# Performance work log

Hardware: AMD Instinct MI355X
Metric: run time of the kernel (lower is better)

## Reference

```python
import jax, jax.numpy as jnp
import numpy as np

EPS = 1e-6
BN_EPS = 1e-5  # torch BatchNorm default eps
B, H, L, D = 4, 8, 128, 64


def _bn(x, gamma, beta, axes):
    # training-mode batchnorm: biased batch stats over `axes`, per-channel (dim 1) affine
    mu = jnp.mean(x, axis=axes, keepdims=True)
    var = jnp.var(x, axis=axes, keepdims=True)
    shape = [1] * x.ndim
    shape[1] = -1
    return (x - mu) * jax.lax.rsqrt(var + BN_EPS) * gamma.reshape(shape) + beta.reshape(shape)


def setup_inputs() -> dict:
    key = jax.random.key(0)
    kq, kk, kv = jax.random.split(key, 3)
    return {
        "Q": jax.random.normal(kq, (B, H, L, D), jnp.float32),
        "K": jax.random.normal(kk, (B, H, L, D), jnp.float32),
        "V": jax.random.uniform(kv, (B, H, L, D), jnp.float32),
        "j_gamma": jnp.ones((H,), jnp.float32),
        "j_beta": jnp.zeros((H,), jnp.float32),
        "h_gamma": jnp.ones((H,), jnp.float32),
        "h_beta": jnp.zeros((H,), jnp.float32),
        "bnH_gamma": jnp.ones((H,), jnp.float32),
        "bnH_beta": jnp.zeros((H,), jnp.float32),
    }


def reference(Q, K, V, j_gamma, j_beta, h_gamma, h_beta, bnH_gamma, bnH_beta):
    # normalize V into a distribution over D, entropy terms
    Vn = V / (jnp.sum(V, axis=-1, keepdims=True) + EPS)
    Vn = jnp.clip(Vn, EPS, 1.0)
    hi = -Vn * jnp.log2(Vn)            # [B,H,L,D]
    h = jnp.sum(hi, axis=-1)           # [B,H,L]

    pQ = jax.nn.softmax(Q, axis=-1)
    pK = jax.nn.softmax(K, axis=-1)
    pQe = pQ[:, :, :, None, :]         # [B,H,L,1,D]
    pKe = pK[:, :, None, :, :]         # [B,H,1,L,D]
    m = 0.5 * (pQe + pKe)              # [B,H,L,L,D] -- dominant intermediate
    kl_q = jnp.sum(pQe * jnp.log2(pQe / (m + EPS) + EPS), axis=-1)  # [B,H,L,L]
    kl_k = jnp.sum(pKe * jnp.log2(pKe / (m + EPS) + EPS), axis=-1)
    J = 0.5 * kl_q + 0.5 * kl_k        # [B,H,L,L]

    # batchnorm only the off-diagonal entries of J (channel = head)
    rows, cols = np.nonzero(~np.eye(L, dtype=bool))
    nd = J[:, :, rows, cols]           # [B,H,L*(L-1)]
    nd = _bn(nd, j_gamma, j_beta, (0, 2))
    J = J.at[:, :, rows, cols].set(nd)

    h = _bn(h, h_gamma, h_beta, (0, 2))

    # QUBO solver stand-in (original detaches + CPU round-trip): binary x per node,
    # greedy heuristic for min x^T J x + h^T x, treated as a constant.
    x = jax.lax.stop_gradient((jnp.sum(J, axis=-1) + h < 0).astype(J.dtype))  # [B,H,L]

    # per-node energy contribution H_i = x_i * ((J x)_i + h_i)
    He = x * (jnp.einsum('bhij,bhj->bhi', J, x) + h)  # [B,H,L]

    Hd = He[..., None] * hi / h[..., None]            # [B,H,L,D]
    Hd = _bn(-Hd, bnH_gamma, bnH_beta, (0, 2, 3))
    return Hd
```

## Files before the change

kernel.cpp:

```cpp
#include <hip/hip_runtime.h>


#define EPS 1e-6f
#define BN_EPS 1e-5f

__global__ void __launch_bounds__(64) k0_rows(
    const float* __restrict__ Q, const float* __restrict__ K,
    const float* __restrict__ V,
    float* __restrict__ pQ, float* __restrict__ pK,
    float* __restrict__ Sq, float* __restrict__ Sk,
    float* __restrict__ hi, float* __restrict__ h_raw)
{
    const int r = blockIdx.x;
    const int lane = threadIdx.x;
    const int base = r * 64 + lane;

    float kk = K[base];
    float m = kk;
    for (int off = 32; off; off >>= 1) m = fmaxf(m, __shfl_xor(m, off));
    float e = __expf(kk - m);
    float s = e;
    for (int off = 32; off; off >>= 1) s += __shfl_xor(s, off);
    const float pk = e * __fdividef(1.0f, s);
    pK[base] = pk;
    float pl = pk * __log2f(pk);
    for (int off = 32; off; off >>= 1) pl += __shfl_xor(pl, off);
    if (lane == 0) Sk[r] = pl;

    float q = Q[base];
    m = q;
    for (int off = 32; off; off >>= 1) m = fmaxf(m, __shfl_xor(m, off));
    e = __expf(q - m);
    s = e;
    for (int off = 32; off; off >>= 1) s += __shfl_xor(s, off);
    const float pq = e * __fdividef(1.0f, s);
    pQ[base] = pq;
    pl = pq * __log2f(pq);
    for (int off = 32; off; off >>= 1) pl += __shfl_xor(pl, off);
    if (lane == 0) Sq[r] = pl;

    float v = V[base];
    s = v;
    for (int off = 32; off; off >>= 1) s += __shfl_xor(s, off);
    float vn = v * __fdividef(1.0f, s + EPS);
    vn = fminf(fmaxf(vn, EPS), 1.0f);
    const float hv = -vn * __log2f(vn);
    hi[base] = hv;
    float hs = hv;
    for (int off = 32; off; off >>= 1) hs += __shfl_xor(hs, off);
    if (lane == 0) h_raw[r] = hs;
}

__global__ void __launch_bounds__(256) ka_J(
    const float* __restrict__ pQ, const float* __restrict__ pK,
    const float* __restrict__ Sq, const float* __restrict__ Sk,
    float* __restrict__ J, float* __restrict__ Sg, float* __restrict__ Dg,
    double* __restrict__ Jpart)
{
    __shared__ float sK[128 * 65];
    __shared__ float sQ[4 * 64];
    __shared__ float sSk[128];
    __shared__ float sSq[4];
    __shared__ double sred[8];
    const int bid = blockIdx.x;
    const int n = bid >> 5;
    const int i0 = (bid & 31) * 4;
    const int tid = threadIdx.x;
    const int wave = tid >> 6, lane = tid & 63;

    const float4* pk4 = (const float4*)(pK + n * 8192);
    #pragma unroll
    for (int v = 0; v < 8; ++v) {
        const int idx = tid + 256 * v;
        const float4 f = pk4[idx];
        float* dst = sK + (idx >> 4) * 65 + (idx & 15) * 4;
        dst[0] = f.x; dst[1] = f.y; dst[2] = f.z; dst[3] = f.w;
    }
    sQ[tid] = pQ[(n * 128 + i0) * 64 + tid];
    if (tid < 128) sSk[tid] = Sk[n * 128 + tid];
    if (tid < 4)   sSq[tid] = Sq[n * 128 + i0 + tid];
    __syncthreads();

    const float* qrow = sQ + wave * 64;
    const float* kp0 = sK + lane * 65;
    const float* kp1 = sK + (lane + 64) * 65;
    float a0 = 0.f, a1 = 0.f;
    #pragma unroll 8
    for (int d = 0; d < 64; ++d) {
        const float qv = qrow[d];
        const float s0v = qv + kp0[d];
        const float s1v = qv + kp1[d];
        a0 += s0v * __log2f(fmaf(0.5f, s0v, EPS));
        a1 += s1v * __log2f(fmaf(0.5f, s1v, EPS));
    }
    const int gi = i0 + wave;
    const float bq = sSq[wave];
    const float J0 = 0.5f * (bq + sSk[lane]      - a0);
    const float J1 = 0.5f * (bq + sSk[lane + 64] - a1);
    const int rbase = (n * 128 + gi) * 128;
    J[rbase + lane] = J0;
    J[rbase + lane + 64] = J1;

    float s0 = J0 + J1;
    for (int off = 32; off; off >>= 1) s0 += __shfl_xor(s0, off);
    const float D = (gi < 64) ? __shfl(J0, gi) : __shfl(J1, gi - 64);
    if (lane == 0) { Sg[n * 128 + gi] = s0; Dg[n * 128 + gi] = D; }

    double ls = 0.0, ls2 = 0.0;
    if (lane != gi)      { ls += J0; ls2 += (double)J0 * (double)J0; }
    if (lane + 64 != gi) { ls += J1; ls2 += (double)J1 * (double)J1; }
    for (int off = 32; off; off >>= 1) {
        ls  += __shfl_xor(ls, off);
        ls2 += __shfl_xor(ls2, off);
    }
    if (lane == 0) { sred[wave] = ls; sred[4 + wave] = ls2; }
    __syncthreads();
    if (tid == 0) {
        Jpart[2 * bid]     = sred[0] + sred[1] + sred[2] + sred[3];
        Jpart[2 * bid + 1] = sred[4] + sred[5] + sred[6] + sred[7];
    }
}

__global__ void __launch_bounds__(256) kc_he(
    const float* __restrict__ J, const float* __restrict__ hi,
    const double* __restrict__ Jpart, const float* __restrict__ h_raw,
    const float* __restrict__ Sg, const float* __restrict__ Dg,
    const float* __restrict__ j_gamma, const float* __restrict__ j_beta,
    const float* __restrict__ h_gamma, const float* __restrict__ h_beta,
    float* __restrict__ t, double* __restrict__ tpart)
{
    __shared__ float sx[128], shbn[128];
    __shared__ double sred[8];
    __shared__ float sprm[5];
    const int bid = blockIdx.x;
    const int n = bid >> 4;
    const int i0 = (bid & 15) * 8;
    const int hh = n & 7;
    const int tid = threadIdx.x;
    const int wave = tid >> 6, lane = tid & 63;

    if (wave == 0) {
        const int p1 = lane, p2 = lane + 64;
        const int pb1 = ((p1 >> 5) * 8 + hh) * 32 + (p1 & 31);
        const int pb2 = ((p2 >> 5) * 8 + hh) * 32 + (p2 & 31);
        double s = Jpart[2 * pb1] + Jpart[2 * pb2];
        double s2 = Jpart[2 * pb1 + 1] + Jpart[2 * pb2 + 1];
        for (int off = 32; off; off >>= 1) {
            s += __shfl_xor(s, off); s2 += __shfl_xor(s2, off);
        }
        if (lane == 0) {
            const double cnt = 65024.0;
            const double mean = s / cnt;
            const double var = s2 / cnt - mean * mean;
            sprm[0] = (float)mean;
            sprm[1] = (float)(1.0 / sqrt(var + (double)BN_EPS));
        }
    }
    {
        double s = 0.0, s2 = 0.0;
        for (int p = tid; p < 512; p += 256) {
            const int b = p >> 7, l = p & 127;
            const float v = h_raw[(b * 8 + hh) * 128 + l];
            s += v; s2 += (double)v * (double)v;
        }
        for (int off = 32; off; off >>= 1) {
            s += __shfl_xor(s, off); s2 += __shfl_xor(s2, off);
        }
        if (lane == 0) { sred[wave] = s; sred[4 + wave] = s2; }
    }
    __syncthreads();
    if (tid == 0) {
        const double hs = sred[0] + sred[1] + sred[2] + sred[3];
        const double hs2 = sred[4] + sred[5] + sred[6] + sred[7];
        const double hm = hs / 512.0;
        const double hvar = hs2 / 512.0 - hm * hm;
        sprm[2] = (float)hm;
        sprm[3] = (float)(1.0 / sqrt(hvar + (double)BN_EPS));
    }
    __syncthreads();
    const float jm = sprm[0], jinv = sprm[1];
    const float hm = sprm[2], hinv = sprm[3];
    const float jg = j_gamma[hh], jb = j_beta[hh];
    if (tid < 128) {
        const int i = tid;
        const float S = Sg[n * 128 + i], D = Dg[n * 128 + i];
        const float hb = (h_raw[n * 128 + i] - hm) * hinv * h_gamma[hh] + h_beta[hh];
        const float rs = jinv * jg * (S - D - 127.0f * jm) + 127.0f * jb + D;
        sx[i] = (rs + hb < 0.0f) ? 1.0f : 0.0f;
        shbn[i] = hb;
    }
    __syncthreads();
    if (wave == 0) {
        float c = sx[lane] + sx[lane + 64];
        for (int off = 32; off; off >>= 1) c += __shfl_xor(c, off);
        if (lane == 0) sprm[4] = c;
    }
    __syncthreads();
    const float C = sprm[4];
    const int rb = wave;
    for (int rr = 0; rr < 2; ++rr) {
        const int i = i0 + rb + 4 * rr;
        const int r = n * 128 + i;
        float tr = J[r * 128 + lane] * sx[lane] + J[r * 128 + 64 + lane] * sx[lane + 64];
        for (int off = 32; off; off >>= 1) tr += __shfl_xor(tr, off);
        const float xi = sx[i], Di = Dg[r];
        const float dot = jinv * jg * (tr - xi * Di - jm * (C - xi))
                        + jb * (C - xi) + xi * Di;
        const float He = xi * (dot + shbn[i]);
        const float tv = -(He * hi[r * 64 + lane] * __fdividef(1.0f, shbn[i]));
        t[r * 64 + lane] = tv;
        double ds = tv, ds2 = (double)tv * (double)tv;
        for (int off = 32; off; off >>= 1) {
            ds += __shfl_xor(ds, off); ds2 += __shfl_xor(ds2, off);
        }
        if (lane == 0) { tpart[2 * r] = ds; tpart[2 * r + 1] = ds2; }
    }
}

__global__ void __launch_bounds__(256) kd_out(
    const double* __restrict__ tpart, const float* __restrict__ t,
    const float* __restrict__ gamma, const float* __restrict__ beta,
    float* __restrict__ out)
{
    __shared__ double sd[256], sd2[256];
    const int bid = blockIdx.x;
    const int tid = threadIdx.x;
    const int g0 = bid * 512;
    const int hh = (g0 >> 13) & 7;
    double s = 0.0, s2 = 0.0;
    for (int p = tid; p < 512; p += 256) {
        const int b = p >> 7, i = p & 127;
        const int r = (b * 8 + hh) * 128 + i;
        s += tpart[2 * r]; s2 += tpart[2 * r + 1];
    }
    sd[tid] = s; sd2[tid] = s2;
    __syncthreads();
    for (int off = 128; off > 0; off >>= 1) {
        if (tid < off) { sd[tid] += sd[tid + off]; sd2[tid] += sd2[tid + off]; }
        __syncthreads();
    }
    const double mean = sd[0] / 32768.0;
    const double var = sd2[0] / 32768.0 - mean * mean;
    const float tm = (float)mean;
    const float tinv = (float)(1.0 / sqrt(var + (double)BN_EPS));
    const float g = gamma[hh], be = beta[hh];
    out[g0 + tid]       = (t[g0 + tid]       - tm) * tinv * g + be;
    out[g0 + 256 + tid] = (t[g0 + 256 + tid] - tm) * tinv * g + be;
}

extern "C" void kernel_launch(void* const* d_in, const int* in_sizes, int n_in,
                              void* d_out, int out_size, void* d_ws, size_t ws_size,
                              hipStream_t stream) {
    (void)in_sizes; (void)n_in; (void)out_size; (void)ws_size;
    const float* Q = (const float*)d_in[0];
    const float* K = (const float*)d_in[1];
    const float* V = (const float*)d_in[2];
    const float* j_gamma = (const float*)d_in[3];
    const float* j_beta  = (const float*)d_in[4];
    const float* h_gamma = (const float*)d_in[5];
    const float* h_beta  = (const float*)d_in[6];
    const float* bnH_gamma = (const float*)d_in[7];
    const float* bnH_beta  = (const float*)d_in[8];
    float* out = (float*)d_out;

    float* w = (float*)d_ws;
    float*  J     = w;
    float*  hi    = w + 524288;
    float*  t     = w + 786432;
    float*  pQ    = w + 1048576;
    float*  pK    = w + 1310720;
    float*  h_raw = w + 1572864;
    float*  Sq    = w + 1576960;
    float*  Sk    = w + 1581056;
    float*  Sg    = w + 1585152;
    float*  Dg    = w + 1589248;
    double* Jpart = (double*)(w + 1593344);
    double* tpart = (double*)(w + 1597440);

    k0_rows<<<4096, 64, 0, stream>>>(Q, K, V, pQ, pK, Sq, Sk, hi, h_raw);
    ka_J<<<1024, 256, 0, stream>>>(pQ, pK, Sq, Sk, J, Sg, Dg, Jpart);
    kc_he<<<512, 256, 0, stream>>>(J, hi, Jpart, h_raw, Sg, Dg,
                                   j_gamma, j_beta, h_gamma, h_beta, t, tpart);
    kd_out<<<512, 256, 0, stream>>>(tpart, t, bnH_gamma, bnH_beta, out);
}
```

Measured before the change: 94.33 us.

## Fuse Q softmax into J kernel and pre-reduce BN partials per block

```diff
diff --git a/kernel.cpp b/kernel.cpp
--- a/kernel.cpp
+++ b/kernel.cpp
@@ -5,10 +5,8 @@
 #define BN_EPS 1e-5f
 
 __global__ void __launch_bounds__(64) k0_rows(
-    const float* __restrict__ Q, const float* __restrict__ K,
-    const float* __restrict__ V,
-    float* __restrict__ pQ, float* __restrict__ pK,
-    float* __restrict__ Sq, float* __restrict__ Sk,
+    const float* __restrict__ K, const float* __restrict__ V,
+    float* __restrict__ pK, float* __restrict__ Sk,
     float* __restrict__ hi, float* __restrict__ h_raw)
 {
     const int r = blockIdx.x;
@@ -27,18 +25,6 @@
     for (int off = 32; off; off >>= 1) pl += __shfl_xor(pl, off);
     if (lane == 0) Sk[r] = pl;
 
-    float q = Q[base];
-    m = q;
-    for (int off = 32; off; off >>= 1) m = fmaxf(m, __shfl_xor(m, off));
-    e = __expf(q - m);
-    s = e;
-    for (int off = 32; off; off >>= 1) s += __shfl_xor(s, off);
-    const float pq = e * __fdividef(1.0f, s);
-    pQ[base] = pq;
-    pl = pq * __log2f(pq);
-    for (int off = 32; off; off >>= 1) pl += __shfl_xor(pl, off);
-    if (lane == 0) Sq[r] = pl;
-
     float v = V[base];
     s = v;
     for (int off = 32; off; off >>= 1) s += __shfl_xor(s, off);
@@ -52,21 +38,33 @@
 }
 
 __global__ void __launch_bounds__(256) ka_J(
-    const float* __restrict__ pQ, const float* __restrict__ pK,
-    const float* __restrict__ Sq, const float* __restrict__ Sk,
+    const float* __restrict__ Q, const float* __restrict__ pK,
+    const float* __restrict__ Sk,
     float* __restrict__ J, float* __restrict__ Sg, float* __restrict__ Dg,
     double* __restrict__ Jpart)
 {
     __shared__ float sK[128 * 65];
     __shared__ float sQ[4 * 64];
     __shared__ float sSk[128];
-    __shared__ float sSq[4];
     __shared__ double sred[8];
     const int bid = blockIdx.x;
     const int n = bid >> 5;
     const int i0 = (bid & 31) * 4;
     const int tid = threadIdx.x;
     const int wave = tid >> 6, lane = tid & 63;
+    const int gi = i0 + wave;
+    const int R = n * 128 + gi;
+
+    float q = Q[R * 64 + lane];
+    float mq = q;
+    for (int off = 32; off; off >>= 1) mq = fmaxf(mq, __shfl_xor(mq, off));
+    float eq = __expf(q - mq);
+    float sq = eq;
+    for (int off = 32; off; off >>= 1) sq += __shfl_xor(sq, off);
+    const float pq = eq * __fdividef(1.0f, sq);
+    sQ[wave * 64 + lane] = pq;
+    float bq = pq * __log2f(pq);
+    for (int off = 32; off; off >>= 1) bq += __shfl_xor(bq, off);
 
     const float4* pk4 = (const float4*)(pK + n * 8192);
     #pragma unroll
@@ -76,9 +74,7 @@
         float* dst = sK + (idx >> 4) * 65 + (idx & 15) * 4;
         dst[0] = f.x; dst[1] = f.y; dst[2] = f.z; dst[3] = f.w;
     }
-    sQ[tid] = pQ[(n * 128 + i0) * 64 + tid];
     if (tid < 128) sSk[tid] = Sk[n * 128 + tid];
-    if (tid < 4)   sSq[tid] = Sq[n * 128 + i0 + tid];
     __syncthreads();
 
     const float* qrow = sQ + wave * 64;
@@ -93,18 +89,16 @@
         a0 += s0v * __log2f(fmaf(0.5f, s0v, EPS));
         a1 += s1v * __log2f(fmaf(0.5f, s1v, EPS));
     }
-    const int gi = i0 + wave;
-    const float bq = sSq[wave];
     const float J0 = 0.5f * (bq + sSk[lane]      - a0);
     const float J1 = 0.5f * (bq + sSk[lane + 64] - a1);
-    const int rbase = (n * 128 + gi) * 128;
+    const int rbase = R * 128;
     J[rbase + lane] = J0;
     J[rbase + lane + 64] = J1;
 
     float s0 = J0 + J1;
     for (int off = 32; off; off >>= 1) s0 += __shfl_xor(s0, off);
     const float D = (gi < 64) ? __shfl(J0, gi) : __shfl(J1, gi - 64);
-    if (lane == 0) { Sg[n * 128 + gi] = s0; Dg[n * 128 + gi] = D; }
+    if (lane == 0) { Sg[R] = s0; Dg[R] = D; }
 
     double ls = 0.0, ls2 = 0.0;
     if (lane != gi)      { ls += J0; ls2 += (double)J0 * (double)J0; }
@@ -127,10 +121,11 @@
     const float* __restrict__ Sg, const float* __restrict__ Dg,
     const float* __restrict__ j_gamma, const float* __restrict__ j_beta,
     const float* __restrict__ h_gamma, const float* __restrict__ h_beta,
-    float* __restrict__ t, double* __restrict__ tpart)
+    float* __restrict__ t, double* __restrict__ tblk)
 {
     __shared__ float sx[128], shbn[128];
     __shared__ double sred[8];
+    __shared__ double st1[4], st2[4];
     __shared__ float sprm[5];
     const int bid = blockIdx.x;
     const int n = bid >> 4;
@@ -198,6 +193,7 @@
     __syncthreads();
     const float C = sprm[4];
     const int rb = wave;
+    double bs = 0.0, bs2 = 0.0;
     for (int rr = 0; rr < 2; ++rr) {
         const int i = i0 + rb + 4 * rr;
         const int r = n * 128 + i;
@@ -213,34 +209,38 @@
         for (int off = 32; off; off >>= 1) {
             ds += __shfl_xor(ds, off); ds2 += __shfl_xor(ds2, off);
         }
-        if (lane == 0) { tpart[2 * r] = ds; tpart[2 * r + 1] = ds2; }
+        if (lane == 0) { bs += ds; bs2 += ds2; }
+    }
+    if (lane == 0) { st1[wave] = bs; st2[wave] = bs2; }
+    __syncthreads();
+    if (tid == 0) {
+        tblk[2 * bid]     = st1[0] + st1[1] + st1[2] + st1[3];
+        tblk[2 * bid + 1] = st2[0] + st2[1] + st2[2] + st2[3];
     }
 }
 
 __global__ void __launch_bounds__(256) kd_out(
-    const double* __restrict__ tpart, const float* __restrict__ t,
+    const double* __restrict__ tblk, const float* __restrict__ t,
     const float* __restrict__ gamma, const float* __restrict__ beta,
     float* __restrict__ out)
 {
-    __shared__ double sd[256], sd2[256];
+    __shared__ double sm[2];
     const int bid = blockIdx.x;
     const int tid = threadIdx.x;
     const int g0 = bid * 512;
     const int hh = (g0 >> 13) & 7;
-    double s = 0.0, s2 = 0.0;
-    for (int p = tid; p < 512; p += 256) {
-        const int b = p >> 7, i = p & 127;
-        const int r = (b * 8 + hh) * 128 + i;
-        s += tpart[2 * r]; s2 += tpart[2 * r + 1];
-    }
-    sd[tid] = s; sd2[tid] = s2;
-    __syncthreads();
-    for (int off = 128; off > 0; off >>= 1) {
-        if (tid < off) { sd[tid] += sd[tid + off]; sd2[tid] += sd2[tid + off]; }
-        __syncthreads();
-    }
-    const double mean = sd[0] / 32768.0;
-    const double var = sd2[0] / 32768.0 - mean * mean;
+    if (tid < 64) {
+        const int b = tid >> 4, tile = tid & 15;
+        const int cb = ((b * 8 + hh) << 4) + tile;
+        double s = tblk[2 * cb], s2 = tblk[2 * cb + 1];
+        for (int off = 32; off; off >>= 1) {
+            s += __shfl_xor(s, off); s2 += __shfl_xor(s2, off);
+        }
+        if (tid == 0) { sm[0] = s; sm[1] = s2; }
+    }
+    __syncthreads();
+    const double mean = sm[0] / 32768.0;
+    const double var = sm[1] / 32768.0 - mean * mean;
     const float tm = (float)mean;
     const float tinv = (float)(1.0 / sqrt(var + (double)BN_EPS));
     const float g = gamma[hh], be = beta[hh];
@@ -267,19 +267,17 @@
     float*  J     = w;
     float*  hi    = w + 524288;
     float*  t     = w + 786432;
-    float*  pQ    = w + 1048576;
     float*  pK    = w + 1310720;
     float*  h_raw = w + 1572864;
-    float*  Sq    = w + 1576960;
     float*  Sk    = w + 1581056;
     float*  Sg    = w + 1585152;
     float*  Dg    = w + 1589248;
     double* Jpart = (double*)(w + 1593344);
-    double* tpart = (double*)(w + 1597440);
-
-    k0_rows<<<4096, 64, 0, stream>>>(Q, K, V, pQ, pK, Sq, Sk, hi, h_raw);
-    ka_J<<<1024, 256, 0, stream>>>(pQ, pK, Sq, Sk, J, Sg, Dg, Jpart);
+    double* tblk  = (double*)(w + 1597440);
+
+    k0_rows<<<4096, 64, 0, stream>>>(K, V, pK, Sk, hi, h_raw);
+    ka_J<<<1024, 256, 0, stream>>>(Q, pK, Sk, J, Sg, Dg, Jpart);
     kc_he<<<512, 256, 0, stream>>>(J, hi, Jpart, h_raw, Sg, Dg,
-                                   j_gamma, j_beta, h_gamma, h_beta, t, tpart);
-    kd_out<<<512, 256, 0, stream>>>(tpart, t, bnH_gamma, bnH_beta, out);
-}
+                                   j_gamma, j_beta, h_gamma, h_beta, t, tblk);
+    kd_out<<<512, 256, 0, stream>>>(tblk, t, bnH_gamma, bnH_beta, out);
+}
```

Measured after the change: 92.68 us. Within noise of the previous version (-1.8%).
